# Performance work log

Hardware: AMD Instinct MI355X
Metric: run time of the kernel (lower is better)

Reference implementation:

```python
import jax, jax.numpy as jnp
import numpy as np

B, C, H, W = 8, 128, 64, 64


def setup_inputs() -> dict:
    key = jax.random.key(0)
    ks = jax.random.split(key, 7)
    query_img = jax.random.normal(ks[0], (B, C, H, W), dtype=jnp.float32)
    key_img = jax.random.normal(ks[1], (B, C, H, W), dtype=jnp.float32)
    value_img = jax.random.normal(ks[2], (B, C, H, W), dtype=jnp.float32)
    # 1x1 conv weights == dense [out, in] matrices (kaiming-ish scale)
    scale = 1.0 / np.sqrt(C)
    Wq = jax.random.normal(ks[3], (C, C), dtype=jnp.float32) * scale
    bq = jax.random.normal(ks[4], (C,), dtype=jnp.float32) * scale
    Wk = jax.random.normal(ks[5], (C, C), dtype=jnp.float32) * scale
    bk = jax.random.normal(ks[6], (C,), dtype=jnp.float32) * scale
    return {"query_img": query_img, "key_img": key_img, "value_img": value_img,
            "Wq": Wq, "bq": bq, "Wk": Wk, "bk": bk}


def reference(query_img, key_img, value_img, Wq, bq, Wk, bk):
    b, c, h, w = query_img.shape
    hw = h * w
    # 1x1 convs as GEMMs -> token-major layout (b, hw, c_out)
    q = jnp.einsum('bchw,oc->bhwo', query_img, Wq).reshape(b, hw, -1) + bq
    k = jnp.einsum('bchw,oc->bohw', key_img, Wk).reshape(b, -1, hw) + bk[None, :, None]
    # scores scaled by sqrt(HW) (faithful: key.size(-1) == h*w in source)
    scores = jnp.einsum('bqc,bck->bqk', q, k) / jnp.sqrt(jnp.float32(hw))
    attn = jax.nn.softmax(scores, axis=-1)  # (b, hw, hw)
    v = value_img.reshape(b, c, hw).transpose(0, 2, 1)  # (b, hw, c)
    out = jnp.einsum('bqk,bkc->bqc', attn, v)  # (b, hw, c)
    out = out.transpose(0, 2, 1).reshape(b, -1, h, w)
    out = out + q.transpose(0, 2, 1).reshape(b, -1, h, w)  # residual from query proj
    return out
```

## Files before the change

kernel.cpp:

```cpp
#include <hip/hip_runtime.h>

#define BB 8
#define CC 128
#define SS 4096
#define KT 64
#define NSPLIT 2
#define HKV (SS / NSPLIT)
#define NIT (HKV / KT)
#define SCALE 0.015625f

typedef __attribute__((ext_vector_type(8))) short sh8;
typedef __attribute__((ext_vector_type(4))) float f32x4;

__device__ __forceinline__ float b2f(unsigned short u) {
    union { unsigned int i; float f; } x; x.i = ((unsigned int)u) << 16; return x.f;
}
__device__ __forceinline__ unsigned short f2b(float f) {
    union { float f; unsigned int i; } x; x.f = f;
    unsigned int r = x.i + 0x7fff + ((x.i >> 16) & 1);
    return (unsigned short)(r >> 16);
}
__device__ __forceinline__ unsigned short rhu(float f) {
    union { float f; unsigned int i; } x; x.f = f;
    return (unsigned short)((x.i + 0x8000) >> 16);
}
__device__ __forceinline__ unsigned int cvtpk(float lo, float hi) {
    unsigned int r;
    asm("v_cvt_pk_bf16_f32 %0, %1, %2" : "=v"(r) : "v"(lo), "v"(hi));
    return r;
}

__device__ __forceinline__ void dma16(const void* g, void* l) {
    __builtin_amdgcn_global_load_lds((const __attribute__((address_space(1))) void*)g,
                                     (__attribute__((address_space(3))) void*)l,
                                     16, 0, 0);
}

__global__ __launch_bounds__(256) void proj_kernel(
    const float* __restrict__ qimg, const float* __restrict__ kimg,
    const float* __restrict__ vimg,
    const float* __restrict__ Wq, const float* __restrict__ Wk,
    const float* __restrict__ bq, const float* __restrict__ bk,
    unsigned short* __restrict__ Qbuf, unsigned short* __restrict__ Kbuf,
    unsigned short* __restrict__ Vbuf)
{
    __shared__ float ilds[128 * 69];

    const int z = blockIdx.z;
    const int b     = blockIdx.y;
    const int stile = blockIdx.x;
    const int tid   = threadIdx.x;

    if (z == 2) {
        const float* src = vimg + (size_t)b * CC * SS + stile * 64;
        unsigned short* dst = Vbuf + (size_t)b * CC * SS + stile * 64;
        #pragma unroll
        for (int i = 0; i < 8; ++i) {
            const int idx = tid + i * 256;
            const int c = idx >> 4, t4 = (idx & 15) * 4;
            float4 v = *(const float4*)(src + (size_t)c * SS + t4);
            ushort4 o;
            o.x = f2b(v.x); o.y = f2b(v.y); o.z = f2b(v.z); o.w = f2b(v.w);
            *(ushort4*)(dst + (size_t)c * SS + t4) = o;
        }
        return;
    }

    const float* img  = (z == 0) ? qimg : kimg;
    const float* Wf   = (z == 0) ? Wq : Wk;
    const float* bias = (z == 0) ? bq : bk;
    unsigned short* outTok = (z == 0) ? Qbuf : Kbuf;

    const int wave = tid >> 6;
    const int lane = tid & 63;
    const int l15  = lane & 15;
    const int quad = lane >> 4;

    const float* gbase = img + (size_t)b * CC * SS + stile * 64;
    #pragma unroll
    for (int i = 0; i < 8; ++i) {
        const int l = tid + 256 * i;
        const int row = l >> 4, col = (l & 15) * 4;
        float4 v = *(const float4*)(gbase + (size_t)row * SS + col);
        float* d = ilds + row * 69 + col;
        d[0] = v.x; d[1] = v.y; d[2] = v.z; d[3] = v.w;
    }
    __syncthreads();

    const int tcol = wave * 16 + l15;
    sh8 a[4];
    #pragma unroll
    for (int kk = 0; kk < 4; ++kk)
        #pragma unroll
        for (int j = 0; j < 8; ++j)
            a[kk][j] = (short)rhu(ilds[(32 * kk + quad * 8 + j) * 69 + tcol]);

    __syncthreads();

    unsigned short* wlds = (unsigned short*)ilds;
    #pragma unroll
    for (int i = 0; i < 8; ++i) {
        const int idx = tid + 256 * i;
        const int row = idx >> 4, ch = idx & 15;
        const float* wp = Wf + (size_t)row * CC + ch * 8;
        float4 w0 = *(const float4*)(wp);
        float4 w1 = *(const float4*)(wp + 4);
        uint4 pk;
        pk.x = cvtpk(w0.x, w0.y); pk.y = cvtpk(w0.z, w0.w);
        pk.z = cvtpk(w1.x, w1.y); pk.w = cvtpk(w1.z, w1.w);
        *(uint4*)((char*)wlds + row * 256 + ((ch ^ (row & 7)) << 4)) = pk;
    }
    __syncthreads();

    f32x4 acc[8];
    #pragma unroll
    for (int nt = 0; nt < 8; ++nt) acc[nt] = (f32x4){0.f, 0.f, 0.f, 0.f};

    #pragma unroll
    for (int nt = 0; nt < 8; ++nt) {
        const int wrow = 16 * nt + l15;
        #pragma unroll
        for (int kk = 0; kk < 4; ++kk) {
            sh8 bf = *(const sh8*)((const char*)wlds + wrow * 256
                                   + (((quad + 4 * kk) ^ (l15 & 7)) << 4));
            acc[nt] = __builtin_amdgcn_mfma_f32_16x16x32_bf16(a[kk], bf, acc[nt], 0, 0, 0);
        }
    }

    __syncthreads();
    unsigned short* oT = (unsigned short*)ilds;
    #pragma unroll
    for (int nt = 0; nt < 8; ++nt) {
        const int o = 16 * nt + l15;
        const float bv = bias[o];
        #pragma unroll
        for (int r = 0; r < 4; ++r) {
            const int sl = wave * 16 + quad * 4 + r;
            oT[sl * 132 + o] = f2b(acc[nt][r] + bv);
        }
    }
    __syncthreads();

    unsigned short* orow = outTok + ((size_t)b * SS + stile * 64) * CC;
    #pragma unroll
    for (int i = 0; i < 8; ++i) {
        const int idx = tid + 256 * i;
        const int s = idx >> 5, o4 = (idx & 31) * 4;
        *(ushort4*)(orow + (size_t)s * CC + o4) = *(const ushort4*)(oT + s * 132 + o4);
    }
}

__global__ __launch_bounds__(256, 2) void attn_kernel(
    const unsigned short* __restrict__ Qbuf,
    const unsigned short* __restrict__ Kbuf,
    const unsigned short* __restrict__ Vbuf,
    float* __restrict__ Oout,
    float* __restrict__ Lsum)
{
    __shared__ __align__(16) unsigned char smem[65536];

    const int tid  = threadIdx.x;
    const int wave = tid >> 6;
    const int lane = tid & 63;
    const int l15  = lane & 15;
    const int quad = lane >> 4;
    const int wgid = blockIdx.x;
    const int b    = wgid & 7;
    const int half = (wgid >> 3) & 1;
    const int qt   = wgid >> 4;
    const int qbase = qt * 128 + wave * 32;
    const int tok0  = half * HKV;

    const unsigned short* kbp = Kbuf + (size_t)b * SS * CC;
    const unsigned short* vbp = Vbuf + (size_t)b * CC * SS;

    sh8 aq[2][4];
    #pragma unroll
    for (int m = 0; m < 2; ++m) {
        const unsigned short* qp = Qbuf + ((size_t)b * SS + qbase + m * 16 + l15) * CC + quad * 8;
        #pragma unroll
        for (int kk = 0; kk < 4; ++kk) aq[m][kk] = *(const sh8*)(qp + 32 * kk);
    }

    int kGO[4], vGO[4];
    #pragma unroll
    for (int j = 0; j < 4; ++j) {
        const int krow = wave * 16 + j * 4 + quad;
        const int sx = (krow & 3) | ((krow >> 1) & 4);
        kGO[j] = krow * 256 + (((lane & 15) ^ sx) << 4);
        const int vrow = (wave * 4 + j) * 8 + (lane >> 3);
        vGO[j] = vrow * 8192 + (((lane & 7) ^ ((lane >> 3) & 7)) << 4);
    }

    int krb[4];
    #pragma unroll
    for (int n = 0; n < 4; ++n)
        krb[n] = (32 * (n >> 1) + 8 * (l15 >> 2) + 4 * (n & 1) + (l15 & 3)) * 256;
    const int krs = l15 & 7;

    f32x4 oacc[2][8];
    #pragma unroll
    for (int m = 0; m < 2; ++m)
        #pragma unroll
        for (int ct = 0; ct < 8; ++ct) oacc[m][ct] = (f32x4){0.f, 0.f, 0.f, 0.f};
    float lsum[2] = {0.f, 0.f};

    const char* gk0 = (const char*)kbp + (size_t)tok0 * 256;
    const char* gv0 = (const char*)vbp + (size_t)tok0 * 2;

    #pragma unroll
    for (int j = 0; j < 4; ++j) {
        dma16(gk0 + kGO[j], smem + (wave * 4 + j) * 1024);
        dma16(gv0 + vGO[j], smem + 32768 + (wave * 4 + j) * 1024);
    }

    for (int it = 0; it < NIT; ++it) {
        unsigned char* kb = smem + ((it & 1) << 14);
        unsigned char* vb = smem + 32768 + ((it & 1) << 14);

        __syncthreads();

        if (it + 1 < NIT) {
            const char* gk = gk0 + (size_t)(it + 1) * KT * 256;
            const char* gv = gv0 + (size_t)(it + 1) * KT * 2;
            unsigned char* kbn = smem + (((it + 1) & 1) << 14);
            unsigned char* vbn = smem + 32768 + (((it + 1) & 1) << 14);
            #pragma unroll
            for (int j = 0; j < 4; ++j) {
                dma16(gk + kGO[j], kbn + (wave * 4 + j) * 1024);
                dma16(gv + vGO[j], vbn + (wave * 4 + j) * 1024);
            }
        }

        f32x4 sacc[2][4];
        #pragma unroll
        for (int m = 0; m < 2; ++m)
            #pragma unroll
            for (int n = 0; n < 4; ++n) sacc[m][n] = (f32x4){0.f, 0.f, 0.f, 0.f};
        __builtin_amdgcn_s_setprio(1);
        #pragma unroll
        for (int n = 0; n < 4; ++n) {
            #pragma unroll
            for (int kk = 0; kk < 4; ++kk) {
                sh8 kf = *(const sh8*)(kb + krb[n] + (((4 * kk + quad) ^ krs) << 4));
                sacc[0][n] = __builtin_amdgcn_mfma_f32_16x16x32_bf16(kf, aq[0][kk], sacc[0][n], 0, 0, 0);
                sacc[1][n] = __builtin_amdgcn_mfma_f32_16x16x32_bf16(kf, aq[1][kk], sacc[1][n], 0, 0, 0);
            }
        }
        __builtin_amdgcn_s_setprio(0);

        union { sh8 v; unsigned int d[4]; } pa[2][2];
        #pragma unroll
        for (int m = 0; m < 2; ++m) {
            float p[4][4];
            #pragma unroll
            for (int n = 0; n < 4; ++n)
                #pragma unroll
                for (int r = 0; r < 4; ++r) {
                    p[n][r] = __expf(sacc[m][n][r] * SCALE);
                    lsum[m] += p[n][r];
                }
            #pragma unroll
            for (int kp = 0; kp < 2; ++kp) {
                pa[m][kp].d[0] = cvtpk(p[2 * kp][0],     p[2 * kp][1]);
                pa[m][kp].d[1] = cvtpk(p[2 * kp][2],     p[2 * kp][3]);
                pa[m][kp].d[2] = cvtpk(p[2 * kp + 1][0], p[2 * kp + 1][1]);
                pa[m][kp].d[3] = cvtpk(p[2 * kp + 1][2], p[2 * kp + 1][3]);
            }
        }

        __builtin_amdgcn_s_setprio(1);
        #pragma unroll
        for (int kp = 0; kp < 2; ++kp) {
            #pragma unroll
            for (int ct = 0; ct < 8; ++ct) {
                sh8 bv = *(const sh8*)(vb + (16 * ct + l15) * 128
                                          + (((kp * 4 + quad) ^ (l15 & 7)) << 4));
                oacc[0][ct] = __builtin_amdgcn_mfma_f32_16x16x32_bf16(pa[0][kp].v, bv, oacc[0][ct], 0, 0, 0);
                oacc[1][ct] = __builtin_amdgcn_mfma_f32_16x16x32_bf16(pa[1][kp].v, bv, oacc[1][ct], 0, 0, 0);
            }
        }
        __builtin_amdgcn_s_setprio(0);
    }

    #pragma unroll
    for (int m = 0; m < 2; ++m) {
        lsum[m] += __shfl_xor(lsum[m], 16, 64);
        lsum[m] += __shfl_xor(lsum[m], 32, 64);
    }
    if (quad == 0) {
        float* lp = Lsum + ((size_t)half * BB + b) * SS + qbase;
        lp[l15]      = lsum[0];
        lp[16 + l15] = lsum[1];
    }

    __syncthreads();

    unsigned short* oT = (unsigned short*)smem;
    #pragma unroll
    for (int m = 0; m < 2; ++m)
        #pragma unroll
        for (int ct = 0; ct < 8; ++ct) {
            const int c  = 16 * ct + l15;
            const int q0 = wave * 32 + m * 16 + quad * 4;
            ushort4 o;
            o.x = rhu(oacc[m][ct][0]); o.y = rhu(oacc[m][ct][1]);
            o.z = rhu(oacc[m][ct][2]); o.w = rhu(oacc[m][ct][3]);
            *(ushort4*)(oT + c * 136 + q0) = o;
        }
    __syncthreads();

    char* ob = (char*)Oout;
    #pragma unroll
    for (int i = 0; i < 16; ++i) {
        const int idx = tid + 256 * i;
        const int c = idx >> 5, q4 = (idx & 31) * 4;
        const size_t rb = ((size_t)(b * CC + c) * SS + (size_t)qt * 128) * 4;
        *(ushort4*)(ob + rb + half * 256 + q4 * 2) = *(const ushort4*)(oT + c * 136 + q4);
    }
}

__global__ __launch_bounds__(256) void combine_kernel(
    const unsigned short* __restrict__ Qbuf,
    const float* __restrict__ Lsum,
    float* __restrict__ out)
{
    __shared__ unsigned short rS[128][132];
    const int b = blockIdx.y, qt = blockIdx.x, tid = threadIdx.x;
    const int lane = tid & 63, wave = tid >> 6;
    const int l31 = lane & 31, hw = lane >> 5;

    const unsigned short* qb = Qbuf + ((size_t)b * SS + qt * 128) * CC;
    #pragma unroll
    for (int i = 0; i < 16; ++i) {
        const int idx = tid + 256 * i;
        const int s = idx >> 5, c4 = (idx & 31) * 4;
        *(ushort4*)(&rS[s][c4]) = *(const ushort4*)(qb + (size_t)s * CC + c4);
    }

    const int s0l = l31 * 4;
    float4 l0 = *(const float4*)(Lsum + (size_t)b * SS + qt * 128 + s0l);
    float4 l1 = *(const float4*)(Lsum + ((size_t)BB + b) * SS + qt * 128 + s0l);
    float rinv[4];
    rinv[0] = 1.f / (l0.x + l1.x); rinv[1] = 1.f / (l0.y + l1.y);
    rinv[2] = 1.f / (l0.z + l1.z); rinv[3] = 1.f / (l0.w + l1.w);
    __syncthreads();

    for (int p = 0; p < 16; ++p) {
        const int c = p * 8 + wave * 2 + hw;
        const size_t rb = (size_t)(b * CC + c) * SS + (size_t)qt * 128;
        ushort4 p0 = *(const ushort4*)((const char*)out + rb * 4 + s0l * 2);
        ushort4 p1 = *(const ushort4*)((const char*)out + rb * 4 + 256 + s0l * 2);
        float4 o;
        o.x = (b2f(p0.x) + b2f(p1.x)) * rinv[0] + b2f(rS[s0l + 0][c]);
        o.y = (b2f(p0.y) + b2f(p1.y)) * rinv[1] + b2f(rS[s0l + 1][c]);
        o.z = (b2f(p0.z) + b2f(p1.z)) * rinv[2] + b2f(rS[s0l + 2][c]);
        o.w = (b2f(p0.w) + b2f(p1.w)) * rinv[3] + b2f(rS[s0l + 3][c]);
        *(float4*)(out + rb + s0l) = o;
    }
}

extern "C" void kernel_launch(void* const* d_in, const int* in_sizes, int n_in,
                              void* d_out, int out_size, void* d_ws, size_t ws_size,
                              hipStream_t stream) {
    const float* qimg = (const float*)d_in[0];
    const float* kimg = (const float*)d_in[1];
    const float* vimg = (const float*)d_in[2];
    const float* Wq   = (const float*)d_in[3];
    const float* bq   = (const float*)d_in[4];
    const float* Wk   = (const float*)d_in[5];
    const float* bk   = (const float*)d_in[6];
    float* out = (float*)d_out;

    unsigned short* Qbuf = (unsigned short*)d_ws;
    unsigned short* Kbuf = Qbuf + (size_t)BB * SS * CC;
    unsigned short* Vbuf = Kbuf + (size_t)BB * SS * CC;
    float* Lsum = (float*)(Vbuf + (size_t)BB * SS * CC);

    proj_kernel<<<dim3(SS / 64, BB, 3), 256, 0, stream>>>(
        qimg, kimg, vimg, Wq, Wk, bq, bk, Qbuf, Kbuf, Vbuf);
    attn_kernel<<<dim3(NSPLIT * BB * (SS / 128)), 256, 0, stream>>>(
        Qbuf, Kbuf, Vbuf, out, Lsum);
    combine_kernel<<<dim3(SS / 128, BB), 256, 0, stream>>>(Qbuf, Lsum, out);
}
```

Measured before the change: 185.0 us.

## Software-pipeline QK of next tile with softmax and PV of current tile

Restructures the attention main loop so the QK^T MFMAs for tile it+1 are issued before the exp/convert and PV MFMAs of tile it, using two alternating score accumulator sets. V moves to triple buffering and loads are prefetched two tiles ahead, which raises LDS to 80 KB per block. The aim is to let MFMA work overlap the VALU-heavy softmax and to hide load latency better. The cost is a larger register footprint and more LDS, which could limit the 2-blocks-per-CU occupancy target or cause spills.

```diff
diff --git a/kernel.cpp b/kernel.cpp
--- a/kernel.cpp
+++ b/kernel.cpp
@@ -157,7 +157,7 @@
     float* __restrict__ Oout,
     float* __restrict__ Lsum)
 {
-    __shared__ __align__(16) unsigned char smem[65536];
+    __shared__ __align__(16) unsigned char smem[81920];
 
     const int tid  = threadIdx.x;
     const int wave = tid >> 6;
@@ -208,48 +208,28 @@
     const char* gk0 = (const char*)kbp + (size_t)tok0 * 256;
     const char* gv0 = (const char*)vbp + (size_t)tok0 * 2;
 
-    #pragma unroll
-    for (int j = 0; j < 4; ++j) {
-        dma16(gk0 + kGO[j], smem + (wave * 4 + j) * 1024);
-        dma16(gv0 + vGO[j], smem + 32768 + (wave * 4 + j) * 1024);
-    }
-
-    for (int it = 0; it < NIT; ++it) {
-        unsigned char* kb = smem + ((it & 1) << 14);
-        unsigned char* vb = smem + 32768 + ((it & 1) << 14);
-
-        __syncthreads();
-
-        if (it + 1 < NIT) {
-            const char* gk = gk0 + (size_t)(it + 1) * KT * 256;
-            const char* gv = gv0 + (size_t)(it + 1) * KT * 2;
-            unsigned char* kbn = smem + (((it + 1) & 1) << 14);
-            unsigned char* vbn = smem + 32768 + (((it + 1) & 1) << 14);
-            #pragma unroll
-            for (int j = 0; j < 4; ++j) {
-                dma16(gk + kGO[j], kbn + (wave * 4 + j) * 1024);
-                dma16(gv + vGO[j], vbn + (wave * 4 + j) * 1024);
-            }
-        }
-
-        f32x4 sacc[2][4];
+    typedef union { sh8 v; unsigned int d[4]; } paU;
+    f32x4 saccA[2][4], saccB[2][4];
+
+    auto QK = [&](int j, f32x4 (&dst)[2][4]) {
+        unsigned char* kb = smem + ((j & 1) << 14);
         #pragma unroll
         for (int m = 0; m < 2; ++m)
             #pragma unroll
-            for (int n = 0; n < 4; ++n) sacc[m][n] = (f32x4){0.f, 0.f, 0.f, 0.f};
+            for (int n = 0; n < 4; ++n) dst[m][n] = (f32x4){0.f, 0.f, 0.f, 0.f};
         __builtin_amdgcn_s_setprio(1);
         #pragma unroll
         for (int n = 0; n < 4; ++n) {
             #pragma unroll
             for (int kk = 0; kk < 4; ++kk) {
                 sh8 kf = *(const sh8*)(kb + krb[n] + (((4 * kk + quad) ^ krs) << 4));
-                sacc[0][n] = __builtin_amdgcn_mfma_f32_16x16x32_bf16(kf, aq[0][kk], sacc[0][n], 0, 0, 0);
-                sacc[1][n] = __builtin_amdgcn_mfma_f32_16x16x32_bf16(kf, aq[1][kk], sacc[1][n], 0, 0, 0);
+                dst[0][n] = __builtin_amdgcn_mfma_f32_16x16x32_bf16(kf, aq[0][kk], dst[0][n], 0, 0, 0);
+                dst[1][n] = __builtin_amdgcn_mfma_f32_16x16x32_bf16(kf, aq[1][kk], dst[1][n], 0, 0, 0);
             }
         }
         __builtin_amdgcn_s_setprio(0);
-
-        union { sh8 v; unsigned int d[4]; } pa[2][2];
+    };
+    auto SM = [&](f32x4 (&src)[2][4], paU (&pa)[2][2]) {
         #pragma unroll
         for (int m = 0; m < 2; ++m) {
             float p[4][4];
@@ -257,7 +237,7 @@
             for (int n = 0; n < 4; ++n)
                 #pragma unroll
                 for (int r = 0; r < 4; ++r) {
-                    p[n][r] = __expf(sacc[m][n][r] * SCALE);
+                    p[n][r] = __expf(src[m][n][r] * SCALE);
                     lsum[m] += p[n][r];
                 }
             #pragma unroll
@@ -268,7 +248,9 @@
                 pa[m][kp].d[3] = cvtpk(p[2 * kp + 1][2], p[2 * kp + 1][3]);
             }
         }
-
+    };
+    auto PV = [&](paU (&pa)[2][2], int vi) {
+        unsigned char* vb = smem + 32768 + vi * 16384;
         __builtin_amdgcn_s_setprio(1);
         #pragma unroll
         for (int kp = 0; kp < 2; ++kp) {
@@ -281,6 +263,50 @@
             }
         }
         __builtin_amdgcn_s_setprio(0);
+    };
+
+    #pragma unroll
+    for (int j = 0; j < 4; ++j) {
+        dma16(gk0 + kGO[j], smem + (wave * 4 + j) * 1024);
+        dma16(gv0 + vGO[j], smem + 32768 + (wave * 4 + j) * 1024);
+    }
+    __syncthreads();
+    {
+        const char* gk = gk0 + (size_t)KT * 256;
+        const char* gv = gv0 + (size_t)KT * 2;
+        #pragma unroll
+        for (int j = 0; j < 4; ++j) {
+            dma16(gk + kGO[j], smem + 16384 + (wave * 4 + j) * 1024);
+            dma16(gv + vGO[j], smem + 49152 + (wave * 4 + j) * 1024);
+        }
+    }
+    QK(0, saccA);
+
+    int vcur = 0;
+    for (int it = 0; it < NIT - 1; ++it) {
+        __syncthreads();
+        const int vdst = (vcur == 0) ? 2 : vcur - 1;
+        if (it + 2 < NIT) {
+            const char* gk = gk0 + (size_t)(it + 2) * KT * 256;
+            const char* gv = gv0 + (size_t)(it + 2) * KT * 2;
+            unsigned char* kbn = smem + ((it & 1) << 14);
+            unsigned char* vbn = smem + 32768 + vdst * 16384;
+            #pragma unroll
+            for (int j = 0; j < 4; ++j) {
+                dma16(gk + kGO[j], kbn + (wave * 4 + j) * 1024);
+                dma16(gv + vGO[j], vbn + (wave * 4 + j) * 1024);
+            }
+        }
+        paU pa[2][2];
+        if ((it + 1) & 1) QK(it + 1, saccB); else QK(it + 1, saccA);
+        if (it & 1)       SM(saccB, pa);   else SM(saccA, pa);
+        PV(pa, vcur);
+        vcur = (vcur == 2) ? 0 : vcur + 1;
+    }
+    {
+        paU pa[2][2];
+        SM(saccB, pa);
+        PV(pa, vcur);
     }
 
     #pragma unroll
```

After: 187.4 us. About the same (+1.3%).
